# Kernel optimization log

Hardware: AMD Instinct MI355X
Metric: run time of the kernel (lower is better)

Reference implementation:

```python
import jax, jax.numpy as jnp
import numpy as np

BUCKET_SIZE = 1_000_000
EMBED_DIM = 128
BATCH = 4096
HIST = 200

# Deterministic on-device stand-in for the md5 bucket hash: a multiplicative
# integer mix (Knuth) followed by mod bucket_size. Same structure as the
# original (arbitrary id -> uniform bucket index); md5 itself is a CPU-side

def hash_buckets(ids, bucket_size):
    mixed = (ids.astype(jnp.uint32) * np.uint32(2654435761))
    return (mixed % np.uint32(bucket_size)).astype(jnp.int32)


def setup_inputs() -> dict:
    key = jax.random.key(0)
    k1, k2 = jax.random.split(key)
    x = jax.random.randint(k1, (BATCH, HIST), 0, 10_000_000, dtype=jnp.int64)
    # Embedding table (nn.Embedding default init ~ N(0,1))
    table = jax.random.normal(k2, (BUCKET_SIZE, EMBED_DIM), dtype=jnp.float32)
    return {"x": x, "table": table}


def reference(x, table):
    # hash ids -> bucket indices, gather embeddings, sum-pool over the id axis
    idx = hash_buckets(x, table.shape[0])            # [B, H] int32
    emb = jnp.take(table, idx, axis=0)               # [B, H, D]
    return emb.sum(axis=1)                           # [B, D]
```

## Files before the change

### kernel.cpp

```cpp
#include <hip/hip_runtime.h>


#define BUCKET        1000000u
#define EMBED_DIM     128
#define HIST          200
#define ROWS_PER_BLK  4

__global__ __launch_bounds__(256, 4)
void hashemb_kernel(const int* __restrict__ x,
                    const float* __restrict__ table,
                    float* __restrict__ out,
                    int batch) {
    __shared__ int sidx[ROWS_PER_BLK * HIST];

    const int row0 = blockIdx.x * ROWS_PER_BLK;

    const int* xblk = x + (size_t)row0 * HIST;
    for (int i = threadIdx.x; i < ROWS_PER_BLK * HIST; i += 256) {
        unsigned int id = (unsigned int)xblk[i];
        sidx[i] = (int)((id * 2654435761u) % BUCKET);
    }
    __syncthreads();

    const int wave = threadIdx.x >> 6;
    const int lane = threadIdx.x & 63;
    const int row  = row0 + wave;
    if (row >= batch) return;

    const int* __restrict__ my = &sidx[wave * HIST];

    float accx = 0.f, accy = 0.f;
    #pragma unroll 8
    for (int h = 0; h < HIST; ++h) {
        const float2 v = *reinterpret_cast<const float2*>(
            table + (size_t)my[h] * EMBED_DIM + lane * 2);
        accx += v.x;
        accy += v.y;
    }

    float2 r;
    r.x = accx;
    r.y = accy;
    *reinterpret_cast<float2*>(out + (size_t)row * EMBED_DIM + lane * 2) = r;
}

extern "C" void kernel_launch(void* const* d_in, const int* in_sizes, int n_in,
                              void* d_out, int out_size, void* d_ws, size_t ws_size,
                              hipStream_t stream) {
    const int*   x     = (const int*)d_in[0];
    const float* table = (const float*)d_in[1];
    float*       out   = (float*)d_out;

    const int batch = in_sizes[0] / HIST;
    const int grid  = (batch + ROWS_PER_BLK - 1) / ROWS_PER_BLK;

    hashemb_kernel<<<grid, 256, 0, stream>>>(x, table, out, batch);
}
```

Before: 66.82 us.

## Bin hashed indices into table quarters so gathers sweep the table in phases

Each row's hashed bucket indices are sorted into one of four range bins with shared-memory atomics, and the wave then gathers bin by bin. The goal is for all concurrently running waves to touch roughly the same quarter of the 512MB table at a time, which should improve L2/MALL or TLB locality. In exchange the kernel adds LDS atomics, a larger shared footprint, and variable-length inner loops. Waves are not synchronized, so whether they actually stay in the same phase is uncertain.

```diff
diff --git a/kernel.cpp b/kernel.cpp
--- a/kernel.cpp
+++ b/kernel.cpp
@@ -5,20 +5,32 @@
 #define EMBED_DIM     128
 #define HIST          200
 #define ROWS_PER_BLK  4
+#define NPASS         4
+#define QRANGE        (BUCKET / NPASS)
 
 __global__ __launch_bounds__(256, 4)
 void hashemb_kernel(const int* __restrict__ x,
                     const float* __restrict__ table,
                     float* __restrict__ out,
                     int batch) {
-    __shared__ int sidx[ROWS_PER_BLK * HIST];
+    __shared__ int lists[ROWS_PER_BLK][NPASS][HIST];
+    __shared__ int cnt[ROWS_PER_BLK][NPASS];
 
     const int row0 = blockIdx.x * ROWS_PER_BLK;
 
+    if (threadIdx.x < ROWS_PER_BLK * NPASS)
+        (&cnt[0][0])[threadIdx.x] = 0;
+    __syncthreads();
+
     const int* xblk = x + (size_t)row0 * HIST;
-    for (int i = threadIdx.x; i < ROWS_PER_BLK * HIST; i += 256) {
-        unsigned int id = (unsigned int)xblk[i];
-        sidx[i] = (int)((id * 2654435761u) % BUCKET);
+    const int nids = min(batch - row0, ROWS_PER_BLK) * HIST;
+    for (int i = threadIdx.x; i < nids; i += 256) {
+        const unsigned int id = (unsigned int)xblk[i];
+        const int idx = (int)((id * 2654435761u) % BUCKET);
+        const int r = i / HIST;
+        const int q = idx / QRANGE;
+        const int pos = atomicAdd(&cnt[r][q], 1);
+        lists[r][q][pos] = idx;
     }
     __syncthreads();
 
@@ -27,21 +39,23 @@
     const int row  = row0 + wave;
     if (row >= batch) return;
 
-    const int* __restrict__ my = &sidx[wave * HIST];
-
     float accx = 0.f, accy = 0.f;
-    #pragma unroll 8
-    for (int h = 0; h < HIST; ++h) {
-        const float2 v = *reinterpret_cast<const float2*>(
-            table + (size_t)my[h] * EMBED_DIM + lane * 2);
-        accx += v.x;
-        accy += v.y;
+    for (int p = 0; p < NPASS; ++p) {
+        const int n = cnt[wave][p];
+        const int* __restrict__ lst = &lists[wave][p][0];
+        #pragma unroll 8
+        for (int h = 0; h < n; ++h) {
+            const float2 v = *reinterpret_cast<const float2*>(
+                table + (size_t)lst[h] * EMBED_DIM + lane * 2);
+            accx += v.x;
+            accy += v.y;
+        }
     }
 
-    float2 r;
-    r.x = accx;
-    r.y = accy;
-    *reinterpret_cast<float2*>(out + (size_t)row * EMBED_DIM + lane * 2) = r;
+    float2 r2;
+    r2.x = accx;
+    r2.y = accy;
+    *reinterpret_cast<float2*>(out + (size_t)row * EMBED_DIM + lane * 2) = r2;
 }
 
 extern "C" void kernel_launch(void* const* d_in, const int* in_sizes, int n_in,
```

Result: slower. 68.63 us (+2.7%).
